# Optimization experiments

Measured on AMD Instinct MI355X. Metric: run time of the kernel, lower is better.

The kernel has to match this reference:

```python
import jax, jax.numpy as jnp
import numpy as np

EPS = 1e-12  # tf.nn.l2_normalize epsilon


def _l2norm(x, axis):
    # tf.nn.l2_normalize: x / sqrt(max(sum(x^2), eps))
    return x * jax.lax.rsqrt(jnp.maximum(jnp.sum(x * x, axis=axis, keepdims=True), EPS))


def setup_inputs() -> dict:
    key = jax.random.key(0)
    k0, k1, k2, k3 = jax.random.split(key, 4)
    B, L, E, C, NG = 128, 1024, 300, 20, 55
    return {
        "x_emb": jax.random.normal(k0, (B, L, E), jnp.float32),
        "x_mask": jnp.ones((B, L), jnp.float32),            # mask_seq = tf.ones(...) in call()
        "W_class": jax.random.normal(k1, (B, C, E), jnp.float32),
        "conv_w": jax.random.normal(k2, (NG, C, C), jnp.float32) * 0.05,  # [width, in=C, out=C]
        "conv_b": jnp.zeros((C,), jnp.float32),
        "W_dis": jax.random.normal(k3, (C, E), jnp.float32) * 0.05,       # 20 per-class 0-layer discriminators
        "b_dis": jnp.zeros((C,), jnp.float32),
    }


def reference(x_emb, x_mask, W_class, conv_w, conv_b, W_dis, b_dis):
    # --- att_emb_ngram_encoder_cnn ---
    x0 = x_emb * x_mask[..., None]                       # b s e (masked word embeddings)
    xn = _l2norm(x0, 2)                                  # b s e
    wn = _l2norm(W_class, 2)                             # b c e (normalize over embed dim)
    G = jnp.einsum('bse,bce->bsc', xn, wn)               # cosine label-word attention, b s c
    # ngram conv smoothing over sequence, SAME padding, relu
    att = jax.lax.conv_general_dilated(
        G, conv_w, window_strides=(1,), padding='SAME',
        dimension_numbers=('NWC', 'WIO', 'NWC')) + conv_b  # b s c
    att = jax.nn.relu(att)
    # partial (masked) softmax over sequence dim
    ew = jnp.exp(att) * x_mask[..., None]                # b s c
    beta = ew / jnp.sum(ew, axis=1, keepdims=True)       # b s c
    # per-class attentive pooling of (unmasked) word embeddings: H_enc b e c
    H = jnp.einsum('bse,bsc->bec', x_emb, beta)
    # --- 20 per-class 0-layer discriminators (dropout is identity at inference) ---
    logits = jnp.einsum('bec,ce->bc', H, W_dis) + b_dis  # b c
    return logits
```

## Files before the change

### kernel.cpp

```cpp
#include <hip/hip_runtime.h>
#include <math.h>

#define B 128
#define L 1024
#define E 300
#define C 20

#define OFF_WNT 0
#define OFF_WDT 768000
#define OFF_SWC 774000
#define OFF_G   796400
#define OFF_D   3417840
#define OFF_S   6039280
#define OFF_T   6041840

__global__ __launch_bounds__(256) void prep_kernel(
    const float* __restrict__ Wc, const float* __restrict__ convw,
    const float* __restrict__ wdis,
    float* __restrict__ wnT, float* __restrict__ wdT,
    float* __restrict__ swc, float* __restrict__ ST)
{
  int t = threadIdx.x;
  int gid = blockIdx.x * 256 + t;

  if (gid < 2 * B * C) ST[gid] = 0.f;

  if (gid < 55 * C * C) {
    int w  = gid / (C * C);
    int r  = gid % (C * C);
    int ci = r / C, co = r % C;
    swc[(((size_t)ci * 4 + co / 5) * 14 + (w >> 2)) * 20 + (co % 5) * 4 + (w & 3)] = convw[gid];
  }
  if (gid < C * C) {
    int ci = gid / C, co = gid % C;
    swc[(((size_t)ci * 4 + co / 5) * 14 + 13) * 20 + (co % 5) * 4 + 3] = 0.f;
  }
  if (gid < 6000) {
    int og = gid / 1500, rem = gid % 1500;
    int kq = rem / 20, i = rem % 20;
    int co = og * 5 + i / 4, q = i & 3;
    wdT[gid] = wdis[(size_t)co * E + kq * 4 + q];
  }

  int row = blockIdx.x * 4 + (t >> 6);
  int ln  = t & 63;
  if (row < B * C) {
    int bb = row / C, c = row % C;
    const float* src = Wc + (size_t)row * E;
    float v[5];
    float ss = 0.f;
    #pragma unroll
    for (int k = 0; k < 5; ++k) {
      int e = ln + 64 * k;
      v[k] = (e < E) ? src[e] : 0.f;
      ss += v[k] * v[k];
    }
    #pragma unroll
    for (int off = 32; off; off >>= 1) ss += __shfl_xor(ss, off, 64);
    float r = rsqrtf(fmaxf(ss, 1e-12f));
    float* dst = wnT + ((size_t)bb * 4 + c / 5) * 1500;
    int cosub = (c % 5) * 4;
    #pragma unroll
    for (int k = 0; k < 5; ++k) {
      int e = ln + 64 * k;
      if (e < E) dst[(e >> 2) * 20 + cosub + (e & 3)] = v[k] * r;
    }
  }
}

__global__ __launch_bounds__(512, 4) void gemm_kernel(
    const float* __restrict__ x, const float* __restrict__ wnT,
    const float* __restrict__ wdT, float* __restrict__ Gt, float* __restrict__ Dt)
{
  __shared__ float xs[32 * 256];

  int t  = threadIdx.x;
  int ln = t & 63;
  int wid  = __builtin_amdgcn_readfirstlane(t >> 6);
  int og   = wid & 3;
  int role = wid >> 2;
  int b  = blockIdx.y;
  int s0 = blockIdx.x * 256;

  const float* wbase = (role == 0) ? (wnT + ((size_t)b * 4 + og) * 1500)
                                   : (wdT + (size_t)og * 1500);

  float acc[5][4];
  #pragma unroll
  for (int c = 0; c < 5; ++c)
    #pragma unroll
    for (int j = 0; j < 4; ++j) acc[c][j] = 0.f;
  float ssq[4] = {0.f, 0.f, 0.f, 0.f};

  for (int chunk = 0; chunk < 10; ++chunk) {
    int k0 = chunk * 32;
    int krem = E - k0; if (krem > 32) krem = 32;

    const float* xb = x + ((size_t)b * L + s0) * E + k0;
    #pragma unroll
    for (int it = 0; it < 4; ++it) {
      int idx = it * 512 + t;
      int row = idx >> 3, col = idx & 7;
      if (col * 4 < krem) {
        float4 f = *(const float4*)(xb + (size_t)row * E + col * 4);
        xs[(col * 4 + 0) * 256 + row] = f.x;
        xs[(col * 4 + 1) * 256 + row] = f.y;
        xs[(col * 4 + 2) * 256 + row] = f.z;
        xs[(col * 4 + 3) * 256 + row] = f.w;
      }
    }
    __syncthreads();

    int nq = krem >> 2;
    #pragma unroll
    for (int kq = 0; kq < 8; ++kq) {
      if (kq < nq) {
        const float* wp = wbase + (chunk * 8 + kq) * 20;
        float w[20];
        #pragma unroll
        for (int i = 0; i < 20; ++i) w[i] = wp[i];
        float4 xk[4];
        #pragma unroll
        for (int q = 0; q < 4; ++q)
          xk[q] = *(const float4*)&xs[(kq * 4 + q) * 256 + ln * 4];
        if (wid == 0) {
          #pragma unroll
          for (int q = 0; q < 4; ++q) {
            const float* xf = (const float*)&xk[q];
            #pragma unroll
            for (int j = 0; j < 4; ++j) ssq[j] = fmaf(xf[j], xf[j], ssq[j]);
          }
        }
        #pragma unroll
        for (int q = 0; q < 4; ++q) {
          const float* xf = (const float*)&xk[q];
          #pragma unroll
          for (int c = 0; c < 5; ++c) {
            float wv = w[c * 4 + q];
            #pragma unroll
            for (int j = 0; j < 4; ++j) acc[c][j] = fmaf(xf[j], wv, acc[c][j]);
          }
        }
      }
    }
    __syncthreads();
  }

  if (wid == 0) {
    #pragma unroll
    for (int j = 0; j < 4; ++j) xs[ln * 4 + j] = rsqrtf(fmaxf(ssq[j], 1e-12f));
  }
  __syncthreads();

  int s = s0 + ln * 4;
  if (role == 0) {
    float4 rv = *(const float4*)&xs[ln * 4];
    const float* rf = (const float*)&rv;
    #pragma unroll
    for (int c = 0; c < 5; ++c) {
      float4 o = { acc[c][0] * rf[0], acc[c][1] * rf[1],
                   acc[c][2] * rf[2], acc[c][3] * rf[3] };
      *(float4*)&Gt[((size_t)b * C + og * 5 + c) * L + s] = o;
    }
  } else {
    #pragma unroll
    for (int c = 0; c < 5; ++c) {
      float4 o = { acc[c][0], acc[c][1], acc[c][2], acc[c][3] };
      *(float4*)&Dt[((size_t)b * C + og * 5 + c) * L + s] = o;
    }
  }
}

#define GP 312
__global__ __launch_bounds__(512, 4) void conv_kernel(
    const float* __restrict__ Gt, const float* __restrict__ Dt,
    const float* __restrict__ swc, const float* __restrict__ convb,
    float* __restrict__ S, float* __restrict__ T)
{
  __shared__ float g_lds[C * GP];

  int t  = threadIdx.x;
  int ln = t & 63;
  int wid = __builtin_amdgcn_readfirstlane(t >> 6);
  int og  = wid & 3;
  int cih = wid >> 2;
  int b  = blockIdx.y;
  int s0 = blockIdx.x * 256;

  for (int c = 0; c < C; ++c)
    for (int h = t; h < GP; h += 512) {
      int s = s0 - 27 + h;
      g_lds[c * GP + h] = (s >= 0 && s < L) ? Gt[((size_t)b * C + c) * L + s] : 0.f;
    }
  __syncthreads();

  float acc[4][5];
  #pragma unroll
  for (int j = 0; j < 4; ++j)
    #pragma unroll
    for (int c = 0; c < 5; ++c) acc[j][c] = 0.f;

  for (int ci = cih * 10; ci < cih * 10 + 10; ++ci) {
    const float* gl = &g_lds[ci * GP + ln * 4];
    const float* wp = swc + ((size_t)ci * 4 + og) * 280;
    float4 g0 = *(const float4*)gl;
    #pragma unroll
    for (int wq = 0; wq < 14; ++wq) {
      float4 g1 = *(const float4*)(gl + wq * 4 + 4);
      float w[20];
      #pragma unroll
      for (int i = 0; i < 20; ++i) w[i] = wp[wq * 20 + i];
      float ga[7] = {g0.x, g0.y, g0.z, g0.w, g1.x, g1.y, g1.z};
      #pragma unroll
      for (int q = 0; q < 4; ++q) {
        #pragma unroll
        for (int j = 0; j < 4; ++j) {
          float gv = ga[q + j];
          #pragma unroll
          for (int c = 0; c < 5; ++c)
            acc[j][c] = fmaf(gv, w[c * 4 + q], acc[j][c]);
        }
      }
      g0 = g1;
    }
  }

  __syncthreads();
  float* scr = g_lds;
  int pr = (og * 64 + ln) * 21;
  if (cih == 1) {
    #pragma unroll
    for (int j = 0; j < 4; ++j)
      #pragma unroll
      for (int c = 0; c < 5; ++c) scr[pr + j * 5 + c] = acc[j][c];
  }
  __syncthreads();

  if (cih == 0) {
    #pragma unroll
    for (int j = 0; j < 4; ++j)
      #pragma unroll
      for (int c = 0; c < 5; ++c) acc[j][c] += scr[pr + j * 5 + c];

    float se[5], st_[5];
    int s = s0 + ln * 4;
    #pragma unroll
    for (int c = 0; c < 5; ++c) {
      float cb = convb[og * 5 + c];
      float4 d4 = *(const float4*)&Dt[((size_t)b * C + og * 5 + c) * L + s];
      const float* df = (const float*)&d4;
      float e0 = 0.f, e1 = 0.f;
      #pragma unroll
      for (int j = 0; j < 4; ++j) {
        float a = acc[j][c] + cb;
        float e = expf(fmaxf(a, 0.f));
        e0 += e;
        e1 += e * df[j];
      }
      se[c] = e0; st_[c] = e1;
    }
    #pragma unroll
    for (int c = 0; c < 5; ++c) {
      #pragma unroll
      for (int off = 32; off; off >>= 1) {
        se[c]  += __shfl_xor(se[c],  off, 64);
        st_[c] += __shfl_xor(st_[c], off, 64);
      }
    }
    if (ln == 0) {
      #pragma unroll
      for (int c = 0; c < 5; ++c) {
        atomicAdd(&S[b * C + og * 5 + c], se[c]);
        atomicAdd(&T[b * C + og * 5 + c], st_[c]);
      }
    }
  }
}

__global__ __launch_bounds__(256) void fin_kernel(
    const float* __restrict__ S, const float* __restrict__ T,
    const float* __restrict__ bdis, float* __restrict__ out)
{
  int i = blockIdx.x * 256 + threadIdx.x;
  if (i < B * C) out[i] = T[i] / S[i] + bdis[i % C];
}

extern "C" void kernel_launch(void* const* d_in, const int* in_sizes, int n_in,
                              void* d_out, int out_size, void* d_ws, size_t ws_size,
                              hipStream_t stream) {
  const float* x_emb = (const float*)d_in[0];
  const float* Wc    = (const float*)d_in[2];
  const float* convw = (const float*)d_in[3];
  const float* convb = (const float*)d_in[4];
  const float* wdis  = (const float*)d_in[5];
  const float* bdis  = (const float*)d_in[6];

  float* ws  = (float*)d_ws;
  float* wnT = ws + OFF_WNT;
  float* wdT = ws + OFF_WDT;
  float* swc = ws + OFF_SWC;
  float* Gt  = ws + OFF_G;
  float* Dt  = ws + OFF_D;
  float* S   = ws + OFF_S;
  float* T   = ws + OFF_T;
  float* out = (float*)d_out;

  prep_kernel<<<640, 256, 0, stream>>>(Wc, convw, wdis, wnT, wdT, swc, S);
  gemm_kernel<<<dim3(L / 256, B), 512, 0, stream>>>(x_emb, wnT, wdT, Gt, Dt);
  conv_kernel<<<dim3(L / 256, B), 512, 0, stream>>>(Gt, Dt, swc, convb, S, T);
  fin_kernel<<<10, 256, 0, stream>>>(S, T, bdis, out);
}
```

Before: 332.3 us.

## Fuse G and D accumulation per wave, swizzle LDS, and split sum-of-squares across waves

The GEMM block drops from 512 to 256 threads. Each wave now computes both the cosine-attention (wn) and discriminator (wd) projections for its class group, so each LDS x-tile read feeds twice as many FMAs. The LDS layout gets an XOR swizzle on rows to reduce bank conflicts, and the per-token sum of squares is spread round-robin across the four waves and then reduced through shared memory instead of being done by one wave. This doubles register accumulators per thread and gives fewer waves per block to hide global-load latency.

Result: slower. 550.0 us (+65.5%).

```diff
diff --git a/kernel.cpp b/kernel.cpp
--- a/kernel.cpp
+++ b/kernel.cpp
@@ -68,7 +68,7 @@
   }
 }
 
-__global__ __launch_bounds__(512, 4) void gemm_kernel(
+__global__ __launch_bounds__(256, 4) void gemm_kernel(
     const float* __restrict__ x, const float* __restrict__ wnT,
     const float* __restrict__ wdT, float* __restrict__ Gt, float* __restrict__ Dt)
 {
@@ -76,20 +76,18 @@
 
   int t  = threadIdx.x;
   int ln = t & 63;
-  int wid  = __builtin_amdgcn_readfirstlane(t >> 6);
-  int og   = wid & 3;
-  int role = wid >> 2;
+  int og = __builtin_amdgcn_readfirstlane(t >> 6);
   int b  = blockIdx.y;
   int s0 = blockIdx.x * 256;
 
-  const float* wbase = (role == 0) ? (wnT + ((size_t)b * 4 + og) * 1500)
-                                   : (wdT + (size_t)og * 1500);
-
-  float acc[5][4];
+  const float* wnbase = wnT + ((size_t)b * 4 + og) * 1500;
+  const float* wdbase = wdT + (size_t)og * 1500;
+
+  float accG[5][4], accD[5][4];
   #pragma unroll
   for (int c = 0; c < 5; ++c)
     #pragma unroll
-    for (int j = 0; j < 4; ++j) acc[c][j] = 0.f;
+    for (int j = 0; j < 4; ++j) { accG[c][j] = 0.f; accD[c][j] = 0.f; }
   float ssq[4] = {0.f, 0.f, 0.f, 0.f};
 
   for (int chunk = 0; chunk < 10; ++chunk) {
@@ -98,32 +96,39 @@
 
     const float* xb = x + ((size_t)b * L + s0) * E + k0;
     #pragma unroll
-    for (int it = 0; it < 4; ++it) {
-      int idx = it * 512 + t;
+    for (int it = 0; it < 8; ++it) {
+      int idx = it * 256 + t;
       int row = idx >> 3, col = idx & 7;
       if (col * 4 < krem) {
         float4 f = *(const float4*)(xb + (size_t)row * E + col * 4);
-        xs[(col * 4 + 0) * 256 + row] = f.x;
-        xs[(col * 4 + 1) * 256 + row] = f.y;
-        xs[(col * 4 + 2) * 256 + row] = f.z;
-        xs[(col * 4 + 3) * 256 + row] = f.w;
+        int r = row ^ ((col & 3) * 8);
+        xs[(col * 4 + 0) * 256 + r] = f.x;
+        xs[(col * 4 + 1) * 256 + r] = f.y;
+        xs[(col * 4 + 2) * 256 + r] = f.z;
+        xs[(col * 4 + 3) * 256 + r] = f.w;
       }
     }
     __syncthreads();
 
     int nq = krem >> 2;
+    bool own_ssq = ((chunk & 3) == og);
     #pragma unroll
     for (int kq = 0; kq < 8; ++kq) {
       if (kq < nq) {
-        const float* wp = wbase + (chunk * 8 + kq) * 20;
-        float w[20];
+        const float* wn_p = wnbase + (chunk * 8 + kq) * 20;
+        const float* wd_p = wdbase + (chunk * 8 + kq) * 20;
+        float4 wn4[5], wd4[5];
         #pragma unroll
-        for (int i = 0; i < 20; ++i) w[i] = wp[i];
+        for (int c = 0; c < 5; ++c) {
+          wn4[c] = ((const float4*)wn_p)[c];
+          wd4[c] = ((const float4*)wd_p)[c];
+        }
+        int rbase = (ln * 4) ^ ((kq & 3) * 8);
         float4 xk[4];
         #pragma unroll
         for (int q = 0; q < 4; ++q)
-          xk[q] = *(const float4*)&xs[(kq * 4 + q) * 256 + ln * 4];
-        if (wid == 0) {
+          xk[q] = *(const float4*)&xs[(kq * 4 + q) * 256 + rbase];
+        if (own_ssq) {
           #pragma unroll
           for (int q = 0; q < 4; ++q) {
             const float* xf = (const float*)&xk[q];
@@ -136,9 +141,13 @@
           const float* xf = (const float*)&xk[q];
           #pragma unroll
           for (int c = 0; c < 5; ++c) {
-            float wv = w[c * 4 + q];
+            float wg = ((const float*)&wn4[c])[q];
+            float wv = ((const float*)&wd4[c])[q];
             #pragma unroll
-            for (int j = 0; j < 4; ++j) acc[c][j] = fmaf(xf[j], wv, acc[c][j]);
+            for (int j = 0; j < 4; ++j) {
+              accG[c][j] = fmaf(xf[j], wg, accG[c][j]);
+              accD[c][j] = fmaf(xf[j], wv, accD[c][j]);
+            }
           }
         }
       }
@@ -146,28 +155,26 @@
     __syncthreads();
   }
 
-  if (wid == 0) {
-    #pragma unroll
-    for (int j = 0; j < 4; ++j) xs[ln * 4 + j] = rsqrtf(fmaxf(ssq[j], 1e-12f));
-  }
+  *(float4*)&xs[og * 256 + ln * 4] = make_float4(ssq[0], ssq[1], ssq[2], ssq[3]);
   __syncthreads();
+  float4 p0 = *(const float4*)&xs[      ln * 4];
+  float4 p1 = *(const float4*)&xs[256 + ln * 4];
+  float4 p2 = *(const float4*)&xs[512 + ln * 4];
+  float4 p3 = *(const float4*)&xs[768 + ln * 4];
+  float rinv[4] = {
+    rsqrtf(fmaxf(p0.x + p1.x + p2.x + p3.x, 1e-12f)),
+    rsqrtf(fmaxf(p0.y + p1.y + p2.y + p3.y, 1e-12f)),
+    rsqrtf(fmaxf(p0.z + p1.z + p2.z + p3.z, 1e-12f)),
+    rsqrtf(fmaxf(p0.w + p1.w + p2.w + p3.w, 1e-12f)) };
 
   int s = s0 + ln * 4;
-  if (role == 0) {
-    float4 rv = *(const float4*)&xs[ln * 4];
-    const float* rf = (const float*)&rv;
-    #pragma unroll
-    for (int c = 0; c < 5; ++c) {
-      float4 o = { acc[c][0] * rf[0], acc[c][1] * rf[1],
-                   acc[c][2] * rf[2], acc[c][3] * rf[3] };
-      *(float4*)&Gt[((size_t)b * C + og * 5 + c) * L + s] = o;
-    }
-  } else {
-    #pragma unroll
-    for (int c = 0; c < 5; ++c) {
-      float4 o = { acc[c][0], acc[c][1], acc[c][2], acc[c][3] };
-      *(float4*)&Dt[((size_t)b * C + og * 5 + c) * L + s] = o;
-    }
+  #pragma unroll
+  for (int c = 0; c < 5; ++c) {
+    float4 g = { accG[c][0] * rinv[0], accG[c][1] * rinv[1],
+                 accG[c][2] * rinv[2], accG[c][3] * rinv[3] };
+    *(float4*)&Gt[((size_t)b * C + og * 5 + c) * L + s] = g;
+    float4 d = { accD[c][0], accD[c][1], accD[c][2], accD[c][3] };
+    *(float4*)&Dt[((size_t)b * C + og * 5 + c) * L + s] = d;
   }
 }
 
@@ -306,7 +313,7 @@
   float* out = (float*)d_out;
 
   prep_kernel<<<640, 256, 0, stream>>>(Wc, convw, wdis, wnT, wdT, swc, S);
-  gemm_kernel<<<dim3(L / 256, B), 512, 0, stream>>>(x_emb, wnT, wdT, Gt, Dt);
+  gemm_kernel<<<dim3(L / 256, B), 256, 0, stream>>>(x_emb, wnT, wdT, Gt, Dt);
   conv_kernel<<<dim3(L / 256, B), 512, 0, stream>>>(Gt, Dt, swc, convb, S, T);
   fin_kernel<<<10, 256, 0, stream>>>(S, T, bdis, out);
 }
```
